# Optimization experiments

Hardware: AMD Instinct MI355X
Metric: run time of the kernel (lower is better)

## Reference

```python
import jax, jax.numpy as jnp
import numpy as np

B, T, D = 4, 4096, 2048
E, C = 8, 512
O = 2048
I = D // E  # expert_in_features = 256


def setup_inputs() -> dict:
    key = jax.random.key(0)
    k1, k2, k3, k4, k5 = jax.random.split(key, 5)
    x = jax.random.normal(k1, (B, T, D), dtype=jnp.float32)
    combine_array = jax.random.uniform(k2, (B, T, E, C), dtype=jnp.float32)
    dispatch_mask = jax.random.uniform(k3, (B, T, E, C), dtype=jnp.float32)
    weight = jax.random.normal(k4, (E, O, I), dtype=jnp.float32) * (1.0 / np.sqrt(I))
    bias = jax.random.normal(k5, (O,), dtype=jnp.float32) * 0.01
    return {"x": x, "combine_array": combine_array, "dispatch_mask": dispatch_mask,
            "weight": weight, "bias": bias}


def reference(x, combine_array, dispatch_mask, weight, bias):
    b, t, d = x.shape
    e, o, i = weight.shape
    # dispatch: one-hot gather of tokens into expert capacity slots
    xr = x.reshape(b, t, e, i)                                   # [B,T,E,I]
    xd = jnp.einsum('btei,btec->beci', xr, dispatch_mask)        # [B,E,C,I]
    # bias homogenization trick: append 1 to features, bias column to weight
    x_homo = jnp.concatenate([xd, jnp.ones_like(xd[..., :1])], axis=-1)       # [B,E,C,I+1]
    b_col = jnp.broadcast_to(bias.reshape(1, o, 1), (e, o, 1))
    w_homo = jnp.concatenate([weight, b_col], axis=-1)                        # [E,O,I+1]
    # per-expert linear then combine scatter back to tokens
    y = jnp.einsum('beci,eoi->beco', x_homo, w_homo)             # [B,E,C,O]
    out = jnp.einsum('beco,btec->bto', y, combine_array)         # [B,T,O]
    return out
```

## Files before the change

### kernel.cpp

```cpp
#include <hip/hip_runtime.h>

typedef float f32x4 __attribute__((ext_vector_type(4)));
typedef short s16x8 __attribute__((ext_vector_type(8)));
typedef short s16x4 __attribute__((ext_vector_type(4)));
typedef unsigned u32x4 __attribute__((ext_vector_type(4)));
typedef unsigned u32x2 __attribute__((ext_vector_type(2)));

#define DEVI __device__ __forceinline__

static constexpr int B_ = 4, T_ = 4096, D_ = 2048, E_ = 8, C_ = 512, O_ = 2048, I_ = 256;
static constexpr size_t XDN = (size_t)B_ * E_ * I_ * C_;

DEVI short f2bf(float f) {
  unsigned u = __builtin_bit_cast(unsigned, f);
  u += 0x7FFFu + ((u >> 16) & 1u);
  return (short)(u >> 16);
}

DEVI unsigned cvtpk(float lo, float hi) {
  unsigned r;
  asm("v_cvt_pk_bf16_f32 %0, %1, %2" : "=v"(r) : "v"(lo), "v"(hi));
  return r;
}

DEVI void gll16(const short* gsrc, short* ldst) {
  __builtin_amdgcn_global_load_lds(
      (const __attribute__((address_space(1))) void*)gsrc,
      (__attribute__((address_space(3))) void*)ldst, 16, 0, 0);
}

__global__ __launch_bounds__(256) void k_prep_wT(const float* __restrict__ w,
                                                 short* __restrict__ wT) {
  int idx = blockIdx.x * 256 + threadIdx.x;
  int o  = idx >> 9;
  int dd = (idx & 511) << 2;
  int e = dd >> 8, i = dd & 255;
  f32x4 v = *(const f32x4*)(w + (((size_t)e * O_ + o) * I_ + i));
  u32x2 p = {cvtpk(v[0], v[1]), cvtpk(v[2], v[3])};
  int dsw = (dd & ~63) | (dd & 7) | ((((dd >> 3) & 7) ^ (o & 7)) << 3);
  *(u32x2*)(wT + (size_t)o * D_ + dsw) = p;
}

__global__ __launch_bounds__(512, 2) void k_gemm1(const float* __restrict__ x,
                                                  const float* __restrict__ disp,
                                                  float* __restrict__ xdP) {
  __shared__ short lXT[128 * 64];
  __shared__ short lDT[256 * 64];
  const int tid = threadIdx.x;
  const int bid = blockIdx.x;
  const int xcd = bid & 7, slot = bid >> 3;
  const int grp = (slot >> 2) * 8 + xcd;
  const int jj = slot & 3;
  const int be = grp >> 1, kc = grp & 1;
  const int mt = jj >> 1, nt = jj & 1;
  const int b = be >> 3, e = be & 7;
  const int lane = tid & 63, wid = tid >> 6;
  const int wm = wid >> 2, wn = wid & 3;
  const int g = lane >> 4, lr = lane & 15;

  const size_t xbase = (size_t)b * T_ * D_ + (size_t)e * I_ + (size_t)mt * 128;
  const size_t dbase = (size_t)b * T_ * (E_ * C_) + (size_t)e * C_ + (size_t)nt * 256;

  const f32x4 z4 = {0.f, 0.f, 0.f, 0.f};
  f32x4 acc[4][4];
#pragma unroll
  for (int i = 0; i < 4; i++)
#pragma unroll
    for (int j = 0; j < 4; j++) acc[i][j] = z4;

  const int xt0 = (tid >> 4) * 2;
  const int xi8 = (tid & 15) * 8;
  const int dt0 = (tid >> 5) * 2;
  const int dc8 = (tid & 31) * 8;
  const int q7 = tid & 7;

  f32x4 xa0, xa1, xb0, xb1;
  f32x4 da[2][4];
  auto loadRegs = [&](int kt) {
    const float* sx = x + xbase + (size_t)(kt + xt0) * D_ + xi8;
    xa0 = *(const f32x4*)sx;
    xa1 = *(const f32x4*)(sx + 4);
    xb0 = *(const f32x4*)(sx + D_);
    xb1 = *(const f32x4*)(sx + D_ + 4);
#pragma unroll
    for (int tt = 0; tt < 2; tt++) {
      const float* sd = disp + dbase + (size_t)(kt + tt * 32 + dt0) * (E_ * C_) + dc8;
      da[tt][0] = *(const f32x4*)sd;
      da[tt][1] = *(const f32x4*)(sd + 4);
      da[tt][2] = *(const f32x4*)(sd + E_ * C_);
      da[tt][3] = *(const f32x4*)(sd + E_ * C_ + 4);
    }
  };
  auto writeLds = [&]() {
#pragma unroll
    for (int j = 0; j < 8; j++) {
      const int i = xi8 + j;
      const int ad = i * 64 + (xt0 ^ ((j ^ q7) << 3));
      float va = (j < 4) ? xa0[j] : xa1[j - 4];
      float vb = (j < 4) ? xb0[j] : xb1[j - 4];
      *(unsigned*)&lXT[ad] = cvtpk(va, vb);
    }
#pragma unroll
    for (int tt = 0; tt < 2; tt++)
#pragma unroll
      for (int j = 0; j < 8; j++) {
        const int c = dc8 + j;
        const int ad = c * 64 + ((tt * 32 + dt0) ^ ((j ^ q7) << 3));
        float ua = (j < 4) ? da[tt][0][j] : da[tt][1][j - 4];
        float ub = (j < 4) ? da[tt][2][j] : da[tt][3][j - 4];
        *(unsigned*)&lDT[ad] = cvtpk(ua, ub);
      }
  };

  const int k0 = kc * 2048, kend = k0 + 2048;
  loadRegs(k0);
  for (int kt = k0; kt < kend; kt += 64) {
    __syncthreads();
    writeLds();
    if (kt + 64 < kend) loadRegs(kt + 64);
    __syncthreads();
#pragma unroll
    for (int kk = 0; kk < 2; kk++) {
      const int tb = kk * 32 + g * 8;
      s16x8 af[4], bfr[4];
#pragma unroll
      for (int mi = 0; mi < 4; mi++) {
        const int r = wm * 64 + mi * 16 + lr;
        const int sws = (((r & 7) ^ ((r >> 3) & 7)) << 3);
        af[mi] = *(const s16x8*)&lXT[r * 64 + (tb ^ sws)];
      }
#pragma unroll
      for (int ni = 0; ni < 4; ni++) {
        const int r = wn * 64 + ni * 16 + lr;
        const int sws = (((r & 7) ^ ((r >> 3) & 7)) << 3);
        bfr[ni] = *(const s16x8*)&lDT[r * 64 + (tb ^ sws)];
      }
#pragma unroll
      for (int mi = 0; mi < 4; mi++)
#pragma unroll
        for (int ni = 0; ni < 4; ni++)
          acc[mi][ni] = __builtin_amdgcn_mfma_f32_16x16x32_bf16(af[mi], bfr[ni], acc[mi][ni], 0, 0, 0);
    }
  }

  float* op = xdP + (size_t)kc * XDN + (size_t)be * I_ * C_;
#pragma unroll
  for (int mi = 0; mi < 4; mi++)
#pragma unroll
    for (int ni = 0; ni < 4; ni++)
#pragma unroll
      for (int r = 0; r < 4; r++) {
        const int ig = mt * 128 + wm * 64 + mi * 16 + g * 4 + r;
        const int cg = nt * 256 + wn * 64 + ni * 16 + lr;
        op[(size_t)ig * C_ + cg] = acc[mi][ni][r];
      }
}

__global__ __launch_bounds__(256) void k_cvt(const float* __restrict__ xdP,
                                             short* __restrict__ xdT) {
  size_t idx = (size_t)blockIdx.x * 256 + threadIdx.x;
  f32x4 a = *(const f32x4*)(xdP + idx * 4);
  f32x4 b = *(const f32x4*)(xdP + XDN + idx * 4);
#pragma unroll
  for (int j = 0; j < 4; j++) a[j] += b[j];
  u32x2 p = {cvtpk(a[0], a[1]), cvtpk(a[2], a[3])};
  *(u32x2*)(xdT + idx * 4) = p;
}

__global__ __launch_bounds__(512, 2) void k_zgemm(const float* __restrict__ comb,
                                                  const short* __restrict__ xdT,
                                                  short* __restrict__ z,
                                                  float* __restrict__ Se) {
  __shared__ short lA[128 * 64];
  __shared__ short lB[256 * 64];
  const int tid = threadIdx.x;
  const int bid = blockIdx.x;
  const int be = bid >> 5, mt = bid & 31;
  const int b = be >> 3, e = be & 7;
  const int lane = tid & 63, wid = tid >> 6;
  const int wm = wid >> 2, wn = wid & 3;
  const int g = lane >> 4, lr = lane & 15;

  const size_t abase = (size_t)b * T_ * (E_ * C_) + (size_t)(mt * 128) * (E_ * C_) + (size_t)e * C_;
  const short* Bsrc = xdT + (size_t)be * I_ * C_;

  float rs[2] = {0.f, 0.f};
  const f32x4 z4 = {0.f, 0.f, 0.f, 0.f};
  f32x4 acc[4][4];
#pragma unroll
  for (int i = 0; i < 4; i++)
#pragma unroll
    for (int j = 0; j < 4; j++) acc[i][j] = z4;

  for (int ct = 0; ct < C_; ct += 64) {
    __syncthreads();
#pragma unroll
    for (int cc = 0; cc < 2; cc++) {
      const int q = tid + 512 * cc;
      const int row = q >> 3;
      const int k8 = (q & 7) << 3;
      const int sw = (row & 7) << 3;
      const float* sa = comb + abase + (size_t)row * (E_ * C_) + ct + k8;
      f32x4 a0 = *(const f32x4*)sa;
      f32x4 a1 = *(const f32x4*)(sa + 4);
      rs[cc] += a0[0] + a0[1] + a0[2] + a0[3] + a1[0] + a1[1] + a1[2] + a1[3];
      u32x4 pw = {cvtpk(a0[0], a0[1]), cvtpk(a0[2], a0[3]),
                  cvtpk(a1[0], a1[1]), cvtpk(a1[2], a1[3])};
      *(u32x4*)&lA[row * 64 + (k8 ^ sw)] = pw;
    }
#pragma unroll
    for (int cc = 0; cc < 4; cc++) {
      const int q = tid + 512 * cc;
      const int row = q >> 3;
      const int k8 = (q & 7) << 3;
      const int sw = (row & 7) << 3;
      s16x8 pb = *(const s16x8*)(Bsrc + (size_t)row * C_ + ct + k8);
      *(s16x8*)&lB[row * 64 + (k8 ^ sw)] = pb;
    }
    __syncthreads();
#pragma unroll
    for (int kk = 0; kk < 2; kk++) {
      const int kb = kk * 32 + g * 8;
      s16x8 af[4], bf[4];
#pragma unroll
      for (int mi = 0; mi < 4; mi++) {
        const int r = wm * 64 + mi * 16 + lr;
        af[mi] = *(const s16x8*)&lA[r * 64 + (kb ^ ((r & 7) << 3))];
      }
#pragma unroll
      for (int ni = 0; ni < 4; ni++) {
        const int r = wn * 64 + ni * 16 + lr;
        bf[ni] = *(const s16x8*)&lB[r * 64 + (kb ^ ((r & 7) << 3))];
      }
#pragma unroll
      for (int mi = 0; mi < 4; mi++)
#pragma unroll
        for (int ni = 0; ni < 4; ni++)
          acc[mi][ni] = __builtin_amdgcn_mfma_f32_16x16x32_bf16(af[mi], bf[ni], acc[mi][ni], 0, 0, 0);
    }
  }
#pragma unroll
  for (int cc = 0; cc < 2; cc++) {
    float v = rs[cc];
    v += __shfl_xor(v, 1);
    v += __shfl_xor(v, 2);
    v += __shfl_xor(v, 4);
    if ((tid & 7) == 0)
      Se[((size_t)b * E_ + e) * T_ + mt * 128 + (tid >> 3) + 64 * cc] = v;
  }
#pragma unroll
  for (int mi = 0; mi < 4; mi++)
#pragma unroll
    for (int ni = 0; ni < 4; ni++)
#pragma unroll
      for (int r = 0; r < 4; r++) {
        const int tg = mt * 128 + wm * 64 + mi * 16 + g * 4 + r;
        const int ig = wn * 64 + ni * 16 + lr;
        const int d = e * I_ + ig;
        const int dsw = (d & ~63) | (d & 7) | ((((d >> 3) & 7) ^ (tg & 7)) << 3);
        z[((size_t)b * T_ + tg) * D_ + dsw] = f2bf(acc[mi][ni][r]);
      }
}

__global__ __launch_bounds__(256) void k_reduceS(const float* __restrict__ Se,
                                                 float* __restrict__ S) {
  int idx = blockIdx.x * 256 + threadIdx.x;
  int b = idx >> 12, t = idx & (T_ - 1);
  float s = 0.f;
#pragma unroll
  for (int e = 0; e < E_; e++) s += Se[((size_t)b * E_ + e) * T_ + t];
  S[idx] = s;
}

__global__ __launch_bounds__(512, 2) void k_outgemm(const short* __restrict__ z,
                                                    const short* __restrict__ wT,
                                                    const float* __restrict__ bias,
                                                    const float* __restrict__ S,
                                                    float* __restrict__ out) {
  __shared__ short lA[2][256 * 64];
  __shared__ short lB[2][256 * 64];
  const int tid = threadIdx.x;
  const int lane = tid & 63, wid = tid >> 6;
  const int wm = wid >> 2, wn = wid & 3;
  const int g = lane >> 4, lr = lane & 15;

  const int bid = blockIdx.x;
  const int swz = (bid & 7) * 64 + (bid >> 3);
  const int mt = swz >> 3, nt = swz & 7;
  const int row0 = mt * 256;
  const int col0 = nt * 256;

  const int srow = (wid << 4) + (lane >> 3);
  const int scol = (lane & 7) << 3;
  const short* Abase = z + (size_t)(row0 + srow) * D_ + scol;
  const short* Bbase = wT + (size_t)(col0 + srow) * D_ + scol;

  const f32x4 zero4 = {0.f, 0.f, 0.f, 0.f};
  f32x4 acc[8][4];
#pragma unroll
  for (int i = 0; i < 8; i++)
#pragma unroll
    for (int j = 0; j < 4; j++) acc[i][j] = zero4;

  s16x8 af[8], bf0[4], bf1[4];
  const int swr = (lr & 7) << 3;

  auto stageA = [&](int sl, int h, int dt) {
    gll16(Abase + (size_t)(h * 128) * D_ + dt, &lA[sl][(h * 128 + wid * 16) * 64]);
    gll16(Abase + (size_t)(h * 128 + 8) * D_ + dt, &lA[sl][(h * 128 + wid * 16 + 8) * 64]);
  };
  auto stageB = [&](int sl, int h, int dt) {
    gll16(Bbase + (size_t)(h * 128) * D_ + dt, &lB[sl][(h * 128 + wid * 16) * 64]);
    gll16(Bbase + (size_t)(h * 128 + 8) * D_ + dt, &lB[sl][(h * 128 + wid * 16 + 8) * 64]);
  };
  auto readA = [&](int sl, int mh) {
#pragma unroll
    for (int mi = 0; mi < 4; mi++) {
      const int r = mh * 128 + wm * 64 + mi * 16 + lr;
#pragma unroll
      for (int ks = 0; ks < 2; ks++)
        af[mi * 2 + ks] = *(const s16x8*)&lA[sl][r * 64 + ((ks * 32 + g * 8) ^ swr)];
    }
  };
  auto readB = [&](int sl, int nh, s16x8* arr) {
#pragma unroll
    for (int ni = 0; ni < 2; ni++) {
      const int r = nh * 128 + wn * 32 + ni * 16 + lr;
#pragma unroll
      for (int ks = 0; ks < 2; ks++)
        arr[ni * 2 + ks] = *(const s16x8*)&lB[sl][r * 64 + ((ks * 32 + g * 8) ^ swr)];
    }
  };
  auto mmaq = [&](int mh, int nh, const s16x8* bb) {
    __builtin_amdgcn_s_setprio(1);
#pragma unroll
    for (int mi = 0; mi < 4; mi++)
#pragma unroll
      for (int ni = 0; ni < 2; ni++)
#pragma unroll
        for (int ks = 0; ks < 2; ks++)
          acc[mh * 4 + mi][nh * 2 + ni] = __builtin_amdgcn_mfma_f32_16x16x32_bf16(
              af[mi * 2 + ks], bb[ni * 2 + ks], acc[mh * 4 + mi][nh * 2 + ni], 0, 0, 0);
    __builtin_amdgcn_s_setprio(0);
  };

#define SYNC(N)                                            \
  asm volatile("s_waitcnt vmcnt(" #N ")" ::: "memory");    \
  __builtin_amdgcn_s_barrier();                            \
  asm volatile("" ::: "memory");

  stageA(0, 0, 0); stageB(0, 0, 0); stageB(0, 1, 0); stageA(0, 1, 0);

  const int NT = D_ / 64;
  for (int t = 0; t < NT - 1; ++t) {
    const int s = t & 1, ns = s ^ 1;
    const int dtn = (t + 1) * 64;
    SYNC(4)
    readA(s, 0); readB(s, 0, bf0);
    stageA(ns, 0, dtn);
    mmaq(0, 0, bf0);
    SYNC(4)
    readB(s, 1, bf1);
    stageB(ns, 0, dtn);
    mmaq(0, 1, bf1);
    SYNC(4)
    readA(s, 1);
    stageB(ns, 1, dtn);
    mmaq(1, 0, bf0);
    stageA(ns, 1, dtn);
    mmaq(1, 1, bf1);
  }
  {
    const int s = (NT - 1) & 1;
    SYNC(4)
    readA(s, 0); readB(s, 0, bf0);
    mmaq(0, 0, bf0);
    SYNC(2)
    readB(s, 1, bf1);
    mmaq(0, 1, bf1);
    SYNC(0)
    readA(s, 1);
    mmaq(1, 0, bf0);
    mmaq(1, 1, bf1);
  }
#undef SYNC

  float bia[4];
#pragma unroll
  for (int nh = 0; nh < 2; nh++)
#pragma unroll
    for (int ni = 0; ni < 2; ni++)
      bia[nh * 2 + ni] = bias[col0 + nh * 128 + wn * 32 + ni * 16 + lr];
#pragma unroll
  for (int mh = 0; mh < 2; mh++)
#pragma unroll
    for (int mi = 0; mi < 4; mi++)
#pragma unroll
      for (int r = 0; r < 4; r++) {
        const int tg = row0 + mh * 128 + wm * 64 + mi * 16 + g * 4 + r;
        const float s = S[tg];
#pragma unroll
        for (int nh = 0; nh < 2; nh++)
#pragma unroll
          for (int ni = 0; ni < 2; ni++) {
            const int og = col0 + nh * 128 + wn * 32 + ni * 16 + lr;
            out[(size_t)tg * O_ + og] = acc[mh * 4 + mi][nh * 2 + ni][r] + bia[nh * 2 + ni] * s;
          }
      }
}

extern "C" void kernel_launch(void* const* d_in, const int* in_sizes, int n_in,
                              void* d_out, int out_size, void* d_ws, size_t ws_size,
                              hipStream_t stream) {
  const float* x    = (const float*)d_in[0];
  const float* comb = (const float*)d_in[1];
  const float* disp = (const float*)d_in[2];
  const float* w    = (const float*)d_in[3];
  const float* bias = (const float*)d_in[4];
  float* out = (float*)d_out;

  char* ws = (char*)d_ws;
  short* wT  = (short*)(ws);
  short* xdT = (short*)(ws + 8388608);
  short* z   = (short*)(ws + 16777216);
  float* xdP = (float*)(ws + 16777216);
  float* Se  = (float*)(ws + 83886080);
  float* S   = (float*)(ws + 84410368);

  k_prep_wT<<<dim3(4096), dim3(256), 0, stream>>>(w, wT);
  k_gemm1<<<dim3(256), dim3(512), 0, stream>>>(x, disp, xdP);
  k_cvt<<<dim3(4096), dim3(256), 0, stream>>>(xdP, xdT);
  k_zgemm<<<dim3(1024), dim3(512), 0, stream>>>(comb, xdT, z, Se);
  k_reduceS<<<dim3(64), dim3(256), 0, stream>>>(Se, S);
  k_outgemm<<<dim3(512), dim3(512), 0, stream>>>(z, wT, bias, S, out);
}
```

Before: 345.9 us.

## Restructure GEMM main loop into 8-phase ping-pong schedule with barrier-fenced MFMA clusters

Replaces the 3-barrier-per-tile double-buffered loop with a manually unrolled two-tile schedule. Each quarter of the MFMA work is wrapped in barriers, and global-to-LDS staging of the next tiles is interleaved at finer granularity, with partial-buffer reuse and a deeper prefetch. The aim is to keep loads in flight longer and to align waves so MFMA and memory phases overlap, in the style of an HipKittens 8-wave ping-pong. The cost is many more barriers per tile and a hard-coded loop count and epilogue, which makes buffer-hazard correctness fragile.

```diff
diff --git a/kernel.cpp b/kernel.cpp
--- a/kernel.cpp
+++ b/kernel.cpp
@@ -344,46 +344,53 @@
     __builtin_amdgcn_s_setprio(0);
   };
 
-#define SYNC(N)                                            \
-  asm volatile("s_waitcnt vmcnt(" #N ")" ::: "memory");    \
-  __builtin_amdgcn_s_barrier();                            \
-  asm volatile("" ::: "memory");
+#define FEN asm volatile("" ::: "memory")
+#define BAR do { FEN; __builtin_amdgcn_s_barrier(); FEN; } while (0)
+#define WV(N) asm volatile("s_waitcnt vmcnt(" #N ")" ::: "memory")
 
   stageA(0, 0, 0); stageB(0, 0, 0); stageB(0, 1, 0); stageA(0, 1, 0);
-
-  const int NT = D_ / 64;
-  for (int t = 0; t < NT - 1; ++t) {
-    const int s = t & 1, ns = s ^ 1;
-    const int dtn = (t + 1) * 64;
-    SYNC(4)
-    readA(s, 0); readB(s, 0, bf0);
-    stageA(ns, 0, dtn);
-    mmaq(0, 0, bf0);
-    SYNC(4)
-    readB(s, 1, bf1);
-    stageB(ns, 0, dtn);
-    mmaq(0, 1, bf1);
-    SYNC(4)
-    readA(s, 1);
-    stageB(ns, 1, dtn);
-    mmaq(1, 0, bf0);
-    stageA(ns, 1, dtn);
+  stageA(1, 0, 64); stageB(1, 0, 64); stageB(1, 1, 64);
+  WV(6); BAR;
+
+  for (int j = 0; j < 15; ++j) {
+    const int d1 = (2 * j + 1) * 64, d2 = (2 * j + 2) * 64, d3 = (2 * j + 3) * 64;
+    readA(0, 0); readB(0, 0, bf0); stageA(1, 1, d1);
+    BAR; mmaq(0, 0, bf0); BAR;
+    readB(0, 1, bf1); stageA(0, 0, d2);
+    BAR; mmaq(0, 1, bf1); BAR;
+    readA(0, 1); stageB(0, 0, d2);
+    BAR; mmaq(1, 0, bf0); BAR;
+    stageB(0, 1, d2); WV(6);
+    BAR; mmaq(1, 1, bf1); BAR;
+    readA(1, 0); readB(1, 0, bf0); stageA(0, 1, d2);
+    BAR; mmaq(0, 0, bf0); BAR;
+    readB(1, 1, bf1); stageA(1, 0, d3);
+    BAR; mmaq(0, 1, bf1); BAR;
+    readA(1, 1); stageB(1, 0, d3);
+    BAR; mmaq(1, 0, bf0); BAR;
+    stageB(1, 1, d3); WV(6);
+    BAR; mmaq(1, 1, bf1); BAR;
+  }
+  {
+    readA(0, 0); readB(0, 0, bf0); stageA(1, 1, 1984);
+    BAR; mmaq(0, 0, bf0); BAR;
+    readB(0, 1, bf1);
+    BAR; mmaq(0, 1, bf1); BAR;
+    readA(0, 1);
+    BAR; mmaq(1, 0, bf0); BAR;
+    WV(4);
+    BAR; mmaq(1, 1, bf1); BAR;
+    readA(1, 0); readB(1, 0, bf0); WV(2);
+    BAR; mmaq(0, 0, bf0); BAR;
+    readB(1, 1, bf1); WV(0);
+    BAR; mmaq(0, 1, bf1); BAR;
+    readA(1, 1);
+    BAR; mmaq(1, 0, bf0); BAR;
     mmaq(1, 1, bf1);
   }
-  {
-    const int s = (NT - 1) & 1;
-    SYNC(4)
-    readA(s, 0); readB(s, 0, bf0);
-    mmaq(0, 0, bf0);
-    SYNC(2)
-    readB(s, 1, bf1);
-    mmaq(0, 1, bf1);
-    SYNC(0)
-    readA(s, 1);
-    mmaq(1, 0, bf0);
-    mmaq(1, 1, bf1);
-  }
-#undef SYNC
+#undef FEN
+#undef BAR
+#undef WV
 
   float bia[4];
 #pragma unroll
```

New measurement: 346.0 us. About the same (+0.0%).
